# Optimization experiments

Hardware: AMD Instinct MI355X
Metric: run time of the kernel (lower is better)

The kernel has to match this reference:

```python
import jax, jax.numpy as jnp
import numpy as np

D_MODEL = 1024
N_HEADS = 16
D_FF = 4096
EPS = 1e-5


def layer_norm(x, gamma, beta):
    mu = jnp.mean(x, axis=-1, keepdims=True)
    var = jnp.mean(jnp.square(x - mu), axis=-1, keepdims=True)
    return (x - mu) * jax.lax.rsqrt(var + EPS) * gamma + beta


def setup_inputs() -> dict:
    key = jax.random.key(0)
    ks = jax.random.split(key, 12)
    C, F = D_MODEL, D_FF
    s = 1.0 / np.sqrt(C)
    sf = 1.0 / np.sqrt(F)
    return {
        "src": jax.random.normal(ks[0], (2, 2048, C), dtype=jnp.float32),
        "w_qkv": jax.random.uniform(ks[1], (3 * C, C), jnp.float32, -s, s),  # qkv_bias=False
        "w_proj": jax.random.uniform(ks[2], (C, C), jnp.float32, -s, s),
        "b_proj": jax.random.uniform(ks[3], (C,), jnp.float32, -s, s),
        "w1": jax.random.uniform(ks[4], (F, C), jnp.float32, -s, s),
        "b1": jax.random.uniform(ks[5], (F,), jnp.float32, -s, s),
        "w2": jax.random.uniform(ks[6], (C, F), jnp.float32, -sf, sf),
        "b2": jax.random.uniform(ks[7], (C,), jnp.float32, -sf, sf),
        "g1": jnp.ones((C,), jnp.float32),
        "be1": jnp.zeros((C,), jnp.float32),
        "g2": jnp.ones((C,), jnp.float32),
        "be2": jnp.zeros((C,), jnp.float32),
    }


def reference(src, w_qkv, w_proj, b_proj, w1, b1, w2, b2, g1, be1, g2, be2):
    B, N, C = src.shape
    H = N_HEADS
    D = C // H
    scale = D ** -0.5
    # --- self-attention (manual QK^T softmax) ---
    qkv = (src @ w_qkv.T).reshape(B, N, 3, H, D).transpose(2, 0, 3, 1, 4)  # [3,B,H,N,D]
    q, k, v = qkv[0], qkv[1], qkv[2]
    attn = jax.nn.softmax(jnp.einsum('bhnd,bhmd->bhnm', q, k) * scale, axis=-1)
    out = jnp.einsum('bhnm,bhmd->bhnd', attn, v).transpose(0, 2, 1, 3).reshape(B, N, C)
    out = out @ w_proj.T + b_proj
    # post-norm residual
    x = layer_norm(src + out, g1, be1)
    # --- FFN ---
    ff = jax.nn.relu(x @ w1.T + b1) @ w2.T + b2
    return layer_norm(x + ff, g2, be2)
```

## Files before the change

kernel.cpp:

```cpp
#include <hip/hip_runtime.h>
#include <hip/hip_bf16.h>
#include <stdint.h>

#define TOKENS 4096
#define SEQ    2048
#define CMODEL 1024
#define HEADS  16
#define HDIM   64
#define DFF    4096
#define NT     (SEQ / 64)

typedef __attribute__((ext_vector_type(8))) short     short8;
typedef __attribute__((ext_vector_type(8))) unsigned short ushort8;
typedef __attribute__((ext_vector_type(4))) unsigned short ushort4v;
typedef __attribute__((ext_vector_type(4))) float     f32x4;

typedef const __attribute__((address_space(1))) void gbl_cvoid;
typedef __attribute__((address_space(3))) void lds_void;

__device__ inline unsigned short f2bf(float f) {
  unsigned int u = __builtin_bit_cast(unsigned int, f);
  u += 0x7fffu + ((u >> 16) & 1u);
  return (unsigned short)(u >> 16);
}
__device__ inline float bf2f(unsigned short h) {
  unsigned int u = ((unsigned int)h) << 16;
  return __builtin_bit_cast(float, u);
}

__device__ inline void gload_lds16(const unsigned short* g, unsigned short* lds) {
  __builtin_amdgcn_global_load_lds((gbl_cvoid*)g, (lds_void*)lds, 16, 0, 0);
}

#define CVT_B0 524288
#define CVT_B1 917504
#define CVT_B2 1048576
#define CVT_B3 1572864
#define CVT_B4 2097152
__global__ __launch_bounds__(256) void k_cvt_all(
    const float* __restrict__ src, const float* __restrict__ wqkv,
    const float* __restrict__ wproj, const float* __restrict__ w1,
    const float* __restrict__ w2,
    unsigned short* __restrict__ o_src, unsigned short* __restrict__ o_wqkv,
    unsigned short* __restrict__ o_wproj, unsigned short* __restrict__ o_w1,
    unsigned short* __restrict__ o_w2)
{
  const int i = blockIdx.x * 256 + threadIdx.x;
  const float* in;
  unsigned short* out;
  int off;
  if (i < CVT_B0)      { in = src;   out = o_src;   off = i; }
  else if (i < CVT_B1) { in = wqkv;  out = o_wqkv;  off = i - CVT_B0; }
  else if (i < CVT_B2) { in = wproj; out = o_wproj; off = i - CVT_B1; }
  else if (i < CVT_B3) { in = w1;    out = o_w1;    off = i - CVT_B2; }
  else                 { in = w2;    out = o_w2;    off = i - CVT_B3; }
  const float4* p = (const float4*)in + 2 * (size_t)off;
  float4 a = p[0], b = p[1];
  ushort8 o;
  o[0] = f2bf(a.x); o[1] = f2bf(a.y); o[2] = f2bf(a.z); o[3] = f2bf(a.w);
  o[4] = f2bf(b.x); o[5] = f2bf(b.y); o[6] = f2bf(b.z); o[7] = f2bf(b.w);
  ((ushort8*)out)[off] = o;
}

template<int EPI>
__global__ __launch_bounds__(256) void k_gemm_bt(
    const unsigned short* __restrict__ A,
    const unsigned short* __restrict__ B,
    unsigned short* __restrict__ Cb,
    float* __restrict__ Cf,
    const float* __restrict__ bias,
    int M, int N, int K, int kspan)
{
  __shared__ unsigned short As[3][128 * 32];
  __shared__ unsigned short Bs[3][128 * 32];
  const int t = threadIdx.x;
  const int lane = t & 63;
  const int w = t >> 6;
  const int wr = w >> 1, wc = w & 1;
  const int nwg = gridDim.x * gridDim.y;
  const int bid = blockIdx.y * gridDim.x + blockIdx.x;
  const int swz = (bid & 7) * (nwg >> 3) + (bid >> 3);
  const int n0 = (swz % gridDim.x) * 128;
  const int m0 = (swz / gridDim.x) * 128;
  const int kbase = blockIdx.z * kspan;

  const int e0 = w * 1024 + lane * 8;
  const int e1 = e0 + 512;
  const int r0 = e0 >> 5, c0 = e0 & 31;
  const int r1 = e1 >> 5, c1 = e1 & 31;

  f32x4 acc[4][4] = {};
  const int lr = lane & 15, lh = lane >> 4;
  const int nkt = kspan >> 5;

  auto stage = [&](int kt, int buf) {
    const int kb = kbase + (kt << 5);
    gload_lds16(A + (size_t)(m0 + r0) * K + kb + c0, &As[buf][w * 1024]);
    gload_lds16(A + (size_t)(m0 + r1) * K + kb + c1, &As[buf][w * 1024 + 512]);
    gload_lds16(B + (size_t)(n0 + r0) * K + kb + c0, &Bs[buf][w * 1024]);
    gload_lds16(B + (size_t)(n0 + r1) * K + kb + c1, &Bs[buf][w * 1024 + 512]);
  };
  stage(0, 0);
  if (nkt > 1) stage(1, 1);

  int buf = 0;
  for (int kt = 0; kt < nkt; ++kt) {
    if (kt + 2 < nkt) {
      const int nb = buf + 2 >= 3 ? buf - 1 : buf + 2;
      stage(kt + 2, nb);
      asm volatile("s_waitcnt vmcnt(8)" ::: "memory");
    } else if (kt + 1 < nkt) {
      asm volatile("s_waitcnt vmcnt(4)" ::: "memory");
    } else {
      asm volatile("s_waitcnt vmcnt(0)" ::: "memory");
    }
    __builtin_amdgcn_s_barrier();
    __builtin_amdgcn_sched_barrier(0);
    short8 af[4], bg[4];
#pragma unroll
    for (int m = 0; m < 4; ++m)
      af[m] = *(const short8*)&As[buf][(wr * 64 + m * 16 + lr) * 32 + lh * 8];
#pragma unroll
    for (int n = 0; n < 4; ++n)
      bg[n] = *(const short8*)&Bs[buf][(wc * 64 + n * 16 + lr) * 32 + lh * 8];
#pragma unroll
    for (int m = 0; m < 4; ++m)
#pragma unroll
      for (int n = 0; n < 4; ++n)
        acc[m][n] = __builtin_amdgcn_mfma_f32_16x16x32_bf16(af[m], bg[n], acc[m][n], 0, 0, 0);
    __builtin_amdgcn_s_barrier();
    __builtin_amdgcn_sched_barrier(0);
    buf = buf + 1 >= 3 ? 0 : buf + 1;
  }

  float* Cfp = (EPI == 4) ? Cf + (size_t)blockIdx.z * ((size_t)M * N) : Cf;
  for (int m = 0; m < 4; ++m) {
    for (int n = 0; n < 4; ++n) {
      const int col = n0 + wc * 64 + n * 16 + lr;
      for (int r = 0; r < 4; ++r) {
        const int row = m0 + wr * 64 + m * 16 + lh * 4 + r;
        const size_t idx = (size_t)row * N + col;
        float v = acc[m][n][r];
        if (EPI == 0) {
          Cb[idx] = f2bf(v);
        } else if (EPI == 2) {
          v += bias[col];
          Cb[idx] = f2bf(v > 0.f ? v : 0.f);
        } else {
          Cfp[idx] = v;
        }
      }
    }
  }
}

__global__ __launch_bounds__(256) void k_attn(
    const unsigned short* __restrict__ qk,
    const unsigned short* __restrict__ vT,
    unsigned short* __restrict__ outb)
{
  __shared__ unsigned short Qs[64 * 64];
  __shared__ unsigned short Ks[2][64 * 64];
  __shared__ unsigned short Vt[2][64 * 64];
  __shared__ unsigned short Ps[4][16 * 72];

  const int t = threadIdx.x, lane = t & 63, w = t >> 6;
  const int bid0 = blockIdx.y * 32 + blockIdx.x;
  const int swz = (bid0 & 7) * 128 + (bid0 >> 3);
  const int bh = swz >> 5;
  const int b = bh >> 4, h = bh & 15;
  const int q0 = (swz & 31) * 64;
  const size_t tokbase = (size_t)b * SEQ;
  const int qoff = h * 64, koff = 1024 + h * 64;
  const size_t vbase = (size_t)(h * 64) * TOKENS + tokbase;
  const int lr = lane & 15, lh = lane >> 4, lh4 = lh * 4;

  const int srow = lane >> 3;
  const int scol = (((lane & 7) ^ srow) & 7) << 3;

  gload_lds16(qk + (tokbase + q0 + w * 16 + srow) * 2048 + qoff + scol, &Qs[w * 1024]);
  gload_lds16(qk + (tokbase + q0 + w * 16 + 8 + srow) * 2048 + qoff + scol, &Qs[w * 1024 + 512]);
  gload_lds16(qk + (tokbase + w * 16 + srow) * 2048 + koff + scol, &Ks[0][w * 1024]);
  gload_lds16(qk + (tokbase + w * 16 + 8 + srow) * 2048 + koff + scol, &Ks[0][w * 1024 + 512]);
  gload_lds16(vT + vbase + (size_t)(w * 16 + srow) * TOKENS + scol, &Vt[0][w * 1024]);
  gload_lds16(vT + vbase + (size_t)(w * 16 + 8 + srow) * TOKENS + scol, &Vt[0][w * 1024 + 512]);
  asm volatile("s_waitcnt vmcnt(0)" ::: "memory");
  __builtin_amdgcn_s_barrier();
  __builtin_amdgcn_sched_barrier(0);

  const int qrow = w * 16 + lr;
  const short8 aq0 = *(const short8*)&Qs[qrow * 64 + (((lh ^ (lr & 7)) & 7) << 3)];
  const short8 aq1 = *(const short8*)&Qs[qrow * 64 + ((((lh + 4) ^ (lr & 7)) & 7) << 3)];

  int koffs0[4], koffs1[4], voffs0[4], voffs1[4];
  for (int nf = 0; nf < 4; ++nf) {
    const int krow = nf * 16 + lr;
    koffs0[nf] = krow * 64 + (((lh ^ (lr & 7)) & 7) << 3);
    koffs1[nf] = krow * 64 + ((((lh + 4) ^ (lr & 7)) & 7) << 3);
    voffs0[nf] = koffs0[nf];
    voffs1[nf] = koffs1[nf];
  }
  const unsigned short* pa0p = &Ps[w][lr * 72 + lh * 8];
  const unsigned short* pa1p = &Ps[w][lr * 72 + 32 + lh * 8];

  float m_run = -1e30f, l_run = 0.f;
  f32x4 oacc[4] = {};
  const float SCL = 0.125f * 1.44269504089f;

#define ATTN_STEP(CUR, KT)                                                        \
  {                                                                               \
    const int ktn = (KT) + 1;                                                     \
    if (ktn < NT) {                                                               \
      gload_lds16(qk + (tokbase + ktn * 64 + w * 16 + srow) * 2048 + koff + scol, \
                  &Ks[1 - (CUR)][w * 1024]);                                      \
      gload_lds16(qk + (tokbase + ktn * 64 + w * 16 + 8 + srow) * 2048 + koff + scol,\
                  &Ks[1 - (CUR)][w * 1024 + 512]);                                \
      gload_lds16(vT + vbase + ktn * 64 + (size_t)(w * 16 + srow) * TOKENS + scol,\
                  &Vt[1 - (CUR)][w * 1024]);                                      \
      gload_lds16(vT + vbase + ktn * 64 + (size_t)(w * 16 + 8 + srow) * TOKENS + scol,\
                  &Vt[1 - (CUR)][w * 1024 + 512]);                                \
      asm volatile("s_waitcnt vmcnt(4)" ::: "memory");                            \
    } else {                                                                      \
      asm volatile("s_waitcnt vmcnt(0)" ::: "memory");                            \
    }                                                                             \
    __builtin_amdgcn_s_barrier();                                                 \
    __builtin_amdgcn_sched_barrier(0);                                            \
    f32x4 sacc[4] = {};                                                           \
    __builtin_amdgcn_s_setprio(1);                                                \
    for (int nf = 0; nf < 4; ++nf) {                                              \
      short8 bk0 = *(const short8*)&Ks[CUR][koffs0[nf]];                          \
      short8 bk1 = *(const short8*)&Ks[CUR][koffs1[nf]];                          \
      sacc[nf] = __builtin_amdgcn_mfma_f32_16x16x32_bf16(bk0, aq0, sacc[nf], 0, 0, 0);\
      sacc[nf] = __builtin_amdgcn_mfma_f32_16x16x32_bf16(bk1, aq1, sacc[nf], 0, 0, 0);\
    }                                                                             \
    __builtin_amdgcn_s_setprio(0);                                                \
    float a0 = fmaxf(fmaxf(sacc[0][0], sacc[0][1]), sacc[0][2]);                  \
    float a1 = fmaxf(fmaxf(sacc[0][3], sacc[1][0]), sacc[1][1]);                  \
    float a2 = fmaxf(fmaxf(sacc[1][2], sacc[1][3]), sacc[2][0]);                  \
    float a3 = fmaxf(fmaxf(sacc[2][1], sacc[2][2]), sacc[2][3]);                  \
    float a4 = fmaxf(fmaxf(sacc[3][0], sacc[3][1]), sacc[3][2]);                  \
    float tm = fmaxf(fmaxf(fmaxf(a0, a1), fmaxf(a2, a3)), fmaxf(a4, sacc[3][3])); \
    tm *= SCL;                                                                    \
    tm = fmaxf(tm, __shfl_xor(tm, 16));                                           \
    tm = fmaxf(tm, __shfl_xor(tm, 32));                                           \
    if (__any(tm > m_run + 5.f)) {               \
      const float mnew = fmaxf(m_run, tm);                                        \
      const float alpha = exp2f(m_run - mnew);                                    \
      m_run = mnew; l_run *= alpha;                                               \
      const float ar0 = __shfl(alpha, lh4 + 0), ar1 = __shfl(alpha, lh4 + 1);     \
      const float ar2 = __shfl(alpha, lh4 + 2), ar3 = __shfl(alpha, lh4 + 3);     \
      for (int nf = 0; nf < 4; ++nf) {                                            \
        oacc[nf][0] *= ar0; oacc[nf][1] *= ar1;                                   \
        oacc[nf][2] *= ar2; oacc[nf][3] *= ar3;                                   \
      }                                                                           \
    }                                                                             \
    float rs = 0.f;                                                               \
    for (int nf = 0; nf < 4; ++nf) {                                              \
      float p0 = exp2f(__builtin_fmaf(sacc[nf][0], SCL, -m_run));                 \
      float p1 = exp2f(__builtin_fmaf(sacc[nf][1], SCL, -m_run));                 \
      float p2 = exp2f(__builtin_fmaf(sacc[nf][2], SCL, -m_run));                 \
      float p3 = exp2f(__builtin_fmaf(sacc[nf][3], SCL, -m_run));                 \
      rs += (p0 + p1) + (p2 + p3);                                                \
      unsigned pk0, pk1;                                                          \
      asm("v_cvt_pk_bf16_f32 %0, %1, %2" : "=v"(pk0) : "v"(p0), "v"(p1));         \
      asm("v_cvt_pk_bf16_f32 %0, %1, %2" : "=v"(pk1) : "v"(p2), "v"(p3));         \
      uint2 pw; pw.x = pk0; pw.y = pk1;                                           \
      *(uint2*)&Ps[w][lr * 72 + nf * 16 + lh4] = pw;                              \
    }                                                                             \
    rs += __shfl_xor(rs, 16);                                                     \
    rs += __shfl_xor(rs, 32);                                                     \
    l_run += rs;                                                                  \
    short8 pa0 = *(const short8*)pa0p;                                            \
    short8 pa1 = *(const short8*)pa1p;                                            \
    __builtin_amdgcn_s_setprio(1);                                                \
    for (int nf = 0; nf < 4; ++nf) {                                              \
      short8 vb0 = *(const short8*)&Vt[CUR][voffs0[nf]];                          \
      short8 vb1 = *(const short8*)&Vt[CUR][voffs1[nf]];                          \
      oacc[nf] = __builtin_amdgcn_mfma_f32_16x16x32_bf16(pa0, vb0, oacc[nf], 0, 0, 0);\
      oacc[nf] = __builtin_amdgcn_mfma_f32_16x16x32_bf16(pa1, vb1, oacc[nf], 0, 0, 0);\
    }                                                                             \
    __builtin_amdgcn_s_setprio(0);                                                \
    __builtin_amdgcn_s_barrier();            \
    __builtin_amdgcn_sched_barrier(0);                                            \
  }

  for (int kt2 = 0; kt2 < NT; kt2 += 2) {
    ATTN_STEP(0, kt2)
    ATTN_STEP(1, kt2 + 1)
  }
#undef ATTN_STEP

  const float lf0 = __shfl(l_run, lh4 + 0);
  const float lf1 = __shfl(l_run, lh4 + 1);
  const float lf2 = __shfl(l_run, lh4 + 2);
  const float lf3 = __shfl(l_run, lh4 + 3);
  const float ri0 = 1.f / lf0, ri1 = 1.f / lf1, ri2 = 1.f / lf2, ri3 = 1.f / lf3;
  for (int nf = 0; nf < 4; ++nf) {
    const int col = h * 64 + nf * 16 + lr;
    const size_t rowb = (tokbase + q0 + w * 16 + lh4) * (size_t)CMODEL + col;
    outb[rowb]               = f2bf(oacc[nf][0] * ri0);
    outb[rowb + CMODEL]      = f2bf(oacc[nf][1] * ri1);
    outb[rowb + 2 * CMODEL]  = f2bf(oacc[nf][2] * ri2);
    outb[rowb + 3 * CMODEL]  = f2bf(oacc[nf][3] * ri3);
  }
}

__global__ __launch_bounds__(256) void k_ln1(
    const float* __restrict__ p,
    const float* __restrict__ src, const float* __restrict__ bias,
    const float* __restrict__ g, const float* __restrict__ b,
    unsigned short* __restrict__ xout)
{
  const int row = blockIdx.x;
  const int t = threadIdx.x;
  const size_t rb = (size_t)row * CMODEL;
  const float4 a0 = ((const float4*)(p + rb))[t];
  const float4 a1 = ((const float4*)(p + (size_t)TOKENS * CMODEL + rb))[t];
  const float4 sv = ((const float4*)(src + rb))[t];
  const float4 bb = ((const float4*)bias)[t];
  float4 v;
  v.x = a0.x + a1.x + sv.x + bb.x;
  v.y = a0.y + a1.y + sv.y + bb.y;
  v.z = a0.z + a1.z + sv.z + bb.z;
  v.w = a0.w + a1.w + sv.w + bb.w;
  float s  = v.x + v.y + v.z + v.w;
  float s2 = v.x * v.x + v.y * v.y + v.z * v.z + v.w * v.w;
  for (int off = 32; off; off >>= 1) { s += __shfl_down(s, off); s2 += __shfl_down(s2, off); }
  __shared__ float red[8];
  __shared__ float stats[2];
  const int wv = t >> 6;
  if ((t & 63) == 0) { red[wv] = s; red[4 + wv] = s2; }
  __syncthreads();
  if (t == 0) {
    float ts  = red[0] + red[1] + red[2] + red[3];
    float ts2 = red[4] + red[5] + red[6] + red[7];
    float mu  = ts * (1.f / CMODEL);
    float var = ts2 * (1.f / CMODEL) - mu * mu;
    stats[0] = mu; stats[1] = rsqrtf(var + 1e-5f);
  }
  __syncthreads();
  const float mu = stats[0], rstd = stats[1];
  float4 gv = ((const float4*)g)[t];
  float4 bv = ((const float4*)b)[t];
  ushort4v o;
  o[0] = f2bf((v.x - mu) * rstd * gv.x + bv.x);
  o[1] = f2bf((v.y - mu) * rstd * gv.y + bv.y);
  o[2] = f2bf((v.z - mu) * rstd * gv.z + bv.z);
  o[3] = f2bf((v.w - mu) * rstd * gv.w + bv.w);
  ((ushort4v*)(xout + rb))[t] = o;
}

__global__ __launch_bounds__(256) void k_ln2(
    const float* __restrict__ q,
    const unsigned short* __restrict__ xres, const float* __restrict__ bias,
    const float* __restrict__ g, const float* __restrict__ b,
    float* __restrict__ out)
{
  const int row = blockIdx.x;
  const int t = threadIdx.x;
  const size_t rb = (size_t)row * CMODEL;
  const float4 a0 = ((const float4*)(q + rb))[t];
  const float4 a1 = ((const float4*)(q + (size_t)TOKENS * CMODEL + rb))[t];
  const ushort4v xv = ((const ushort4v*)(xres + rb))[t];
  const float4 bb = ((const float4*)bias)[t];
  float4 v;
  v.x = a0.x + a1.x + bf2f(xv[0]) + bb.x;
  v.y = a0.y + a1.y + bf2f(xv[1]) + bb.y;
  v.z = a0.z + a1.z + bf2f(xv[2]) + bb.z;
  v.w = a0.w + a1.w + bf2f(xv[3]) + bb.w;
  float s  = v.x + v.y + v.z + v.w;
  float s2 = v.x * v.x + v.y * v.y + v.z * v.z + v.w * v.w;
  for (int off = 32; off; off >>= 1) { s += __shfl_down(s, off); s2 += __shfl_down(s2, off); }
  __shared__ float red[8];
  __shared__ float stats[2];
  const int wv = t >> 6;
  if ((t & 63) == 0) { red[wv] = s; red[4 + wv] = s2; }
  __syncthreads();
  if (t == 0) {
    float ts  = red[0] + red[1] + red[2] + red[3];
    float ts2 = red[4] + red[5] + red[6] + red[7];
    float mu  = ts * (1.f / CMODEL);
    float var = ts2 * (1.f / CMODEL) - mu * mu;
    stats[0] = mu; stats[1] = rsqrtf(var + 1e-5f);
  }
  __syncthreads();
  const float mu = stats[0], rstd = stats[1];
  float4 gv = ((const float4*)g)[t];
  float4 bv = ((const float4*)b)[t];
  float4 o;
  o.x = (v.x - mu) * rstd * gv.x + bv.x;
  o.y = (v.y - mu) * rstd * gv.y + bv.y;
  o.z = (v.z - mu) * rstd * gv.z + bv.z;
  o.w = (v.w - mu) * rstd * gv.w + bv.w;
  ((float4*)(out + rb))[t] = o;
}

extern "C" void kernel_launch(void* const* d_in, const int* in_sizes, int n_in,
                              void* d_out, int out_size, void* d_ws, size_t ws_size,
                              hipStream_t stream) {
  const float* src    = (const float*)d_in[0];
  const float* w_qkv  = (const float*)d_in[1];
  const float* w_proj = (const float*)d_in[2];
  const float* b_proj = (const float*)d_in[3];
  const float* w1     = (const float*)d_in[4];
  const float* b1     = (const float*)d_in[5];
  const float* w2     = (const float*)d_in[6];
  const float* b2     = (const float*)d_in[7];
  const float* g1     = (const float*)d_in[8];
  const float* be1    = (const float*)d_in[9];
  const float* g2     = (const float*)d_in[10];
  const float* be2    = (const float*)d_in[11];
  float* out = (float*)d_out;

  char* ws = (char*)d_ws;
  size_t off = 0;
  auto alloc = [&](size_t bytes) -> void* {
    void* p = ws + off;
    off += (bytes + 255) & ~(size_t)255;
    return p;
  };
  unsigned short* src_bf   = (unsigned short*)alloc((size_t)TOKENS * CMODEL * 2);
  unsigned short* wqkv_bf  = (unsigned short*)alloc((size_t)3 * CMODEL * CMODEL * 2);
  unsigned short* wproj_bf = (unsigned short*)alloc((size_t)CMODEL * CMODEL * 2);
  unsigned short* w1_bf    = (unsigned short*)alloc((size_t)DFF * CMODEL * 2);
  unsigned short* w2_bf    = (unsigned short*)alloc((size_t)CMODEL * DFF * 2);
  unsigned short* x_bf     = (unsigned short*)alloc((size_t)TOKENS * CMODEL * 2);
  unsigned short* h_bf     = (unsigned short*)alloc((size_t)TOKENS * DFF * 2);
  char* regionR = (char*)alloc((size_t)64 * 1024 * 1024);
  unsigned short* qk_bf    = (unsigned short*)regionR;
  unsigned short* vT_bf    = (unsigned short*)(regionR + (size_t)TOKENS * 2048 * 2);
  unsigned short* attno_bf = (unsigned short*)(regionR + (size_t)TOKENS * 2048 * 2
                                                       + (size_t)CMODEL * TOKENS * 2);
  float*          p_proj   = (float*)(regionR + (size_t)TOKENS * 2048 * 2
                                              + (size_t)CMODEL * TOKENS * 2
                                              + (size_t)TOKENS * CMODEL * 2);
  float*          p_ffn2   = (float*)regionR;

  k_cvt_all<<<CVT_B4 / 256, 256, 0, stream>>>(src, w_qkv, w_proj, w1, w2,
      src_bf, wqkv_bf, wproj_bf, w1_bf, w2_bf);
  k_gemm_bt<0><<<dim3(2048 / 128, TOKENS / 128), 256, 0, stream>>>(
      src_bf, wqkv_bf, qk_bf, nullptr, nullptr, TOKENS, 2048, CMODEL, CMODEL);
  k_gemm_bt<0><<<dim3(TOKENS / 128, CMODEL / 128), 256, 0, stream>>>(
      wqkv_bf + (size_t)2048 * CMODEL, src_bf, vT_bf, nullptr, nullptr,
      CMODEL, TOKENS, CMODEL, CMODEL);
  k_attn<<<dim3(SEQ / 64, 2 * HEADS), 256, 0, stream>>>(qk_bf, vT_bf, attno_bf);
  k_gemm_bt<4><<<dim3(CMODEL / 128, TOKENS / 128, 2), 256, 0, stream>>>(
      attno_bf, wproj_bf, nullptr, p_proj, nullptr, TOKENS, CMODEL, CMODEL, CMODEL / 2);
  k_ln1<<<TOKENS, 256, 0, stream>>>(p_proj, src, b_proj, g1, be1, x_bf);
  k_gemm_bt<2><<<dim3(DFF / 128, TOKENS / 128), 256, 0, stream>>>(
      x_bf, w1_bf, h_bf, nullptr, b1, TOKENS, DFF, CMODEL, CMODEL);
  k_gemm_bt<4><<<dim3(CMODEL / 128, TOKENS / 128, 2), 256, 0, stream>>>(
      h_bf, w2_bf, nullptr, p_ffn2, nullptr, TOKENS, CMODEL, DFF, DFF / 2);
  k_ln2<<<TOKENS, 256, 0, stream>>>(p_ffn2, x_bf, b2, g2, be2, out);
}
```

Before: 400.7 us.

## Replace split-K GEMMs with BN=64 tiles and fuse bias+residual into epilogue

The N=1024 GEMMs (attention projection and FFN down) drop split-K over z=2 and use 128x64 tiles instead, which keeps the grid at 512 blocks. Bias and residual addition move into the GEMM epilogue so the layernorm kernels only read one fp32 buffer, and ln1 and ln2 become a single templated kernel. In attention the Q staging buffer is reused for the P tile to reduce LDS use. This removes the second partial-sum write and read, at the cost of narrower tiles with lower reuse and a full-K loop per block.

```diff
diff --git a/kernel.cpp b/kernel.cpp
--- a/kernel.cpp
+++ b/kernel.cpp
@@ -62,17 +62,20 @@
   ((ushort8*)out)[off] = o;
 }
 
-template<int EPI>
+template<int EPI, int BN>
 __global__ __launch_bounds__(256) void k_gemm_bt(
     const unsigned short* __restrict__ A,
     const unsigned short* __restrict__ B,
     unsigned short* __restrict__ Cb,
     float* __restrict__ Cf,
     const float* __restrict__ bias,
-    int M, int N, int K, int kspan)
+    const float* __restrict__ resf,
+    const unsigned short* __restrict__ resb,
+    int M, int N, int K)
 {
+  constexpr int NF = BN >> 5;
   __shared__ unsigned short As[3][128 * 32];
-  __shared__ unsigned short Bs[3][128 * 32];
+  __shared__ unsigned short Bs[3][BN * 32];
   const int t = threadIdx.x;
   const int lane = t & 63;
   const int w = t >> 6;
@@ -80,25 +83,30 @@
   const int nwg = gridDim.x * gridDim.y;
   const int bid = blockIdx.y * gridDim.x + blockIdx.x;
   const int swz = (bid & 7) * (nwg >> 3) + (bid >> 3);
-  const int n0 = (swz % gridDim.x) * 128;
+  const int n0 = (swz % gridDim.x) * BN;
   const int m0 = (swz / gridDim.x) * 128;
-  const int kbase = blockIdx.z * kspan;
 
   const int e0 = w * 1024 + lane * 8;
   const int e1 = e0 + 512;
   const int r0 = e0 >> 5, c0 = e0 & 31;
   const int r1 = e1 >> 5, c1 = e1 & 31;
-
-  f32x4 acc[4][4] = {};
+  const int eB = w * 512 + lane * 8;
+  const int rB = eB >> 5, cB = eB & 31;
+
+  f32x4 acc[4][NF] = {};
   const int lr = lane & 15, lh = lane >> 4;
-  const int nkt = kspan >> 5;
+  const int nkt = K >> 5;
 
   auto stage = [&](int kt, int buf) {
-    const int kb = kbase + (kt << 5);
+    const int kb = kt << 5;
     gload_lds16(A + (size_t)(m0 + r0) * K + kb + c0, &As[buf][w * 1024]);
     gload_lds16(A + (size_t)(m0 + r1) * K + kb + c1, &As[buf][w * 1024 + 512]);
-    gload_lds16(B + (size_t)(n0 + r0) * K + kb + c0, &Bs[buf][w * 1024]);
-    gload_lds16(B + (size_t)(n0 + r1) * K + kb + c1, &Bs[buf][w * 1024 + 512]);
+    if constexpr (BN == 128) {
+      gload_lds16(B + (size_t)(n0 + r0) * K + kb + c0, &Bs[buf][w * 1024]);
+      gload_lds16(B + (size_t)(n0 + r1) * K + kb + c1, &Bs[buf][w * 1024 + 512]);
+    } else {
+      gload_lds16(B + (size_t)(n0 + rB) * K + kb + cB, &Bs[buf][w * 512]);
+    }
   };
   stage(0, 0);
   if (nkt > 1) stage(1, 1);
@@ -108,46 +116,49 @@
     if (kt + 2 < nkt) {
       const int nb = buf + 2 >= 3 ? buf - 1 : buf + 2;
       stage(kt + 2, nb);
-      asm volatile("s_waitcnt vmcnt(8)" ::: "memory");
+      if constexpr (BN == 128) asm volatile("s_waitcnt vmcnt(8)" ::: "memory");
+      else                     asm volatile("s_waitcnt vmcnt(6)" ::: "memory");
     } else if (kt + 1 < nkt) {
-      asm volatile("s_waitcnt vmcnt(4)" ::: "memory");
+      if constexpr (BN == 128) asm volatile("s_waitcnt vmcnt(4)" ::: "memory");
+      else                     asm volatile("s_waitcnt vmcnt(3)" ::: "memory");
     } else {
       asm volatile("s_waitcnt vmcnt(0)" ::: "memory");
     }
     __builtin_amdgcn_s_barrier();
     __builtin_amdgcn_sched_barrier(0);
-    short8 af[4], bg[4];
+    short8 af[4], bg[NF];
 #pragma unroll
     for (int m = 0; m < 4; ++m)
       af[m] = *(const short8*)&As[buf][(wr * 64 + m * 16 + lr) * 32 + lh * 8];
 #pragma unroll
-    for (int n = 0; n < 4; ++n)
-      bg[n] = *(const short8*)&Bs[buf][(wc * 64 + n * 16 + lr) * 32 + lh * 8];
+    for (int n = 0; n < NF; ++n)
+      bg[n] = *(const short8*)&Bs[buf][(wc * (BN / 2) + n * 16 + lr) * 32 + lh * 8];
 #pragma unroll
     for (int m = 0; m < 4; ++m)
 #pragma unroll
-      for (int n = 0; n < 4; ++n)
+      for (int n = 0; n < NF; ++n)
         acc[m][n] = __builtin_amdgcn_mfma_f32_16x16x32_bf16(af[m], bg[n], acc[m][n], 0, 0, 0);
     __builtin_amdgcn_s_barrier();
     __builtin_amdgcn_sched_barrier(0);
     buf = buf + 1 >= 3 ? 0 : buf + 1;
   }
 
-  float* Cfp = (EPI == 4) ? Cf + (size_t)blockIdx.z * ((size_t)M * N) : Cf;
   for (int m = 0; m < 4; ++m) {
-    for (int n = 0; n < 4; ++n) {
-      const int col = n0 + wc * 64 + n * 16 + lr;
+    for (int n = 0; n < NF; ++n) {
+      const int col = n0 + wc * (BN / 2) + n * 16 + lr;
       for (int r = 0; r < 4; ++r) {
         const int row = m0 + wr * 64 + m * 16 + lh * 4 + r;
         const size_t idx = (size_t)row * N + col;
         float v = acc[m][n][r];
         if (EPI == 0) {
           Cb[idx] = f2bf(v);
+        } else if (EPI == 1) {
+          Cf[idx] = v + bias[col] + resf[idx];
         } else if (EPI == 2) {
           v += bias[col];
           Cb[idx] = f2bf(v > 0.f ? v : 0.f);
         } else {
-          Cfp[idx] = v;
+          Cf[idx] = v + bias[col] + bf2f(resb[idx]);
         }
       }
     }
@@ -159,10 +170,9 @@
     const unsigned short* __restrict__ vT,
     unsigned short* __restrict__ outb)
 {
-  __shared__ unsigned short Qs[64 * 64];
   __shared__ unsigned short Ks[2][64 * 64];
   __shared__ unsigned short Vt[2][64 * 64];
-  __shared__ unsigned short Ps[4][16 * 72];
+  __shared__ unsigned short QPs[4 * 1024];
 
   const int t = threadIdx.x, lane = t & 63, w = t >> 6;
   const int bid0 = blockIdx.y * 32 + blockIdx.x;
@@ -178,8 +188,8 @@
   const int srow = lane >> 3;
   const int scol = (((lane & 7) ^ srow) & 7) << 3;
 
-  gload_lds16(qk + (tokbase + q0 + w * 16 + srow) * 2048 + qoff + scol, &Qs[w * 1024]);
-  gload_lds16(qk + (tokbase + q0 + w * 16 + 8 + srow) * 2048 + qoff + scol, &Qs[w * 1024 + 512]);
+  gload_lds16(qk + (tokbase + q0 + w * 16 + srow) * 2048 + qoff + scol, &QPs[w * 1024]);
+  gload_lds16(qk + (tokbase + q0 + w * 16 + 8 + srow) * 2048 + qoff + scol, &QPs[w * 1024 + 512]);
   gload_lds16(qk + (tokbase + w * 16 + srow) * 2048 + koff + scol, &Ks[0][w * 1024]);
   gload_lds16(qk + (tokbase + w * 16 + 8 + srow) * 2048 + koff + scol, &Ks[0][w * 1024 + 512]);
   gload_lds16(vT + vbase + (size_t)(w * 16 + srow) * TOKENS + scol, &Vt[0][w * 1024]);
@@ -188,20 +198,20 @@
   __builtin_amdgcn_s_barrier();
   __builtin_amdgcn_sched_barrier(0);
 
-  const int qrow = w * 16 + lr;
-  const short8 aq0 = *(const short8*)&Qs[qrow * 64 + (((lh ^ (lr & 7)) & 7) << 3)];
-  const short8 aq1 = *(const short8*)&Qs[qrow * 64 + ((((lh + 4) ^ (lr & 7)) & 7) << 3)];
-
-  int koffs0[4], koffs1[4], voffs0[4], voffs1[4];
+  const short8 aq0 = *(const short8*)&QPs[w * 1024 + lr * 64 + (((lh ^ (lr & 7)) & 7) << 3)];
+  const short8 aq1 = *(const short8*)&QPs[w * 1024 + lr * 64 + ((((lh + 4) ^ (lr & 7)) & 7) << 3)];
+
+  int koffs0[4], koffs1[4];
   for (int nf = 0; nf < 4; ++nf) {
     const int krow = nf * 16 + lr;
     koffs0[nf] = krow * 64 + (((lh ^ (lr & 7)) & 7) << 3);
     koffs1[nf] = krow * 64 + ((((lh + 4) ^ (lr & 7)) & 7) << 3);
-    voffs0[nf] = koffs0[nf];
-    voffs1[nf] = koffs1[nf];
-  }
-  const unsigned short* pa0p = &Ps[w][lr * 72 + lh * 8];
-  const unsigned short* pa1p = &Ps[w][lr * 72 + 32 + lh * 8];
+  }
+  const unsigned short* pa0p = &QPs[w * 1024 + lr * 64 + (((lh ^ (lr & 7)) & 7) << 3)];
+  const unsigned short* pa1p = &QPs[w * 1024 + lr * 64 + ((((4 + lh) ^ (lr & 7)) & 7) << 3)];
+  int pwr[4];
+  for (int nf = 0; nf < 4; ++nf)
+    pwr[nf] = w * 1024 + lr * 64 + ((((nf * 2 + (lh4 >> 3)) ^ (lr & 7)) & 7) << 3) + (lh4 & 7);
 
   float m_run = -1e30f, l_run = 0.f;
   f32x4 oacc[4] = {};
@@ -265,7 +275,7 @@
       asm("v_cvt_pk_bf16_f32 %0, %1, %2" : "=v"(pk0) : "v"(p0), "v"(p1));         \
       asm("v_cvt_pk_bf16_f32 %0, %1, %2" : "=v"(pk1) : "v"(p2), "v"(p3));         \
       uint2 pw; pw.x = pk0; pw.y = pk1;                                           \
-      *(uint2*)&Ps[w][lr * 72 + nf * 16 + lh4] = pw;                              \
+      *(uint2*)&QPs[pwr[nf]] = pw;                                                \
     }                                                                             \
     rs += __shfl_xor(rs, 16);                                                     \
     rs += __shfl_xor(rs, 32);                                                     \
@@ -274,8 +284,8 @@
     short8 pa1 = *(const short8*)pa1p;                                            \
     __builtin_amdgcn_s_setprio(1);                                                \
     for (int nf = 0; nf < 4; ++nf) {                                              \
-      short8 vb0 = *(const short8*)&Vt[CUR][voffs0[nf]];                          \
-      short8 vb1 = *(const short8*)&Vt[CUR][voffs1[nf]];                          \
+      short8 vb0 = *(const short8*)&Vt[CUR][koffs0[nf]];                          \
+      short8 vb1 = *(const short8*)&Vt[CUR][koffs1[nf]];                          \
       oacc[nf] = __builtin_amdgcn_mfma_f32_16x16x32_bf16(pa0, vb0, oacc[nf], 0, 0, 0);\
       oacc[nf] = __builtin_amdgcn_mfma_f32_16x16x32_bf16(pa1, vb1, oacc[nf], 0, 0, 0);\
     }                                                                             \
@@ -305,24 +315,15 @@
   }
 }
 
-__global__ __launch_bounds__(256) void k_ln1(
-    const float* __restrict__ p,
-    const float* __restrict__ src, const float* __restrict__ bias,
+template<int OUT_BF>
+__global__ __launch_bounds__(256) void k_ln(const float* __restrict__ in,
     const float* __restrict__ g, const float* __restrict__ b,
-    unsigned short* __restrict__ xout)
+    float* __restrict__ outf, unsigned short* __restrict__ outb)
 {
   const int row = blockIdx.x;
   const int t = threadIdx.x;
-  const size_t rb = (size_t)row * CMODEL;
-  const float4 a0 = ((const float4*)(p + rb))[t];
-  const float4 a1 = ((const float4*)(p + (size_t)TOKENS * CMODEL + rb))[t];
-  const float4 sv = ((const float4*)(src + rb))[t];
-  const float4 bb = ((const float4*)bias)[t];
-  float4 v;
-  v.x = a0.x + a1.x + sv.x + bb.x;
-  v.y = a0.y + a1.y + sv.y + bb.y;
-  v.z = a0.z + a1.z + sv.z + bb.z;
-  v.w = a0.w + a1.w + sv.w + bb.w;
+  const float4* x4 = (const float4*)(in + (size_t)row * CMODEL);
+  float4 v = x4[t];
   float s  = v.x + v.y + v.z + v.w;
   float s2 = v.x * v.x + v.y * v.y + v.z * v.z + v.w * v.w;
   for (int off = 32; off; off >>= 1) { s += __shfl_down(s, off); s2 += __shfl_down(s2, off); }
@@ -342,57 +343,17 @@
   const float mu = stats[0], rstd = stats[1];
   float4 gv = ((const float4*)g)[t];
   float4 bv = ((const float4*)b)[t];
-  ushort4v o;
-  o[0] = f2bf((v.x - mu) * rstd * gv.x + bv.x);
-  o[1] = f2bf((v.y - mu) * rstd * gv.y + bv.y);
-  o[2] = f2bf((v.z - mu) * rstd * gv.z + bv.z);
-  o[3] = f2bf((v.w - mu) * rstd * gv.w + bv.w);
-  ((ushort4v*)(xout + rb))[t] = o;
-}
-
-__global__ __launch_bounds__(256) void k_ln2(
-    const float* __restrict__ q,
-    const unsigned short* __restrict__ xres, const float* __restrict__ bias,
-    const float* __restrict__ g, const float* __restrict__ b,
-    float* __restrict__ out)
-{
-  const int row = blockIdx.x;
-  const int t = threadIdx.x;
-  const size_t rb = (size_t)row * CMODEL;
-  const float4 a0 = ((const float4*)(q + rb))[t];
-  const float4 a1 = ((const float4*)(q + (size_t)TOKENS * CMODEL + rb))[t];
-  const ushort4v xv = ((const ushort4v*)(xres + rb))[t];
-  const float4 bb = ((const float4*)bias)[t];
-  float4 v;
-  v.x = a0.x + a1.x + bf2f(xv[0]) + bb.x;
-  v.y = a0.y + a1.y + bf2f(xv[1]) + bb.y;
-  v.z = a0.z + a1.z + bf2f(xv[2]) + bb.z;
-  v.w = a0.w + a1.w + bf2f(xv[3]) + bb.w;
-  float s  = v.x + v.y + v.z + v.w;
-  float s2 = v.x * v.x + v.y * v.y + v.z * v.z + v.w * v.w;
-  for (int off = 32; off; off >>= 1) { s += __shfl_down(s, off); s2 += __shfl_down(s2, off); }
-  __shared__ float red[8];
-  __shared__ float stats[2];
-  const int wv = t >> 6;
-  if ((t & 63) == 0) { red[wv] = s; red[4 + wv] = s2; }
-  __syncthreads();
-  if (t == 0) {
-    float ts  = red[0] + red[1] + red[2] + red[3];
-    float ts2 = red[4] + red[5] + red[6] + red[7];
-    float mu  = ts * (1.f / CMODEL);
-    float var = ts2 * (1.f / CMODEL) - mu * mu;
-    stats[0] = mu; stats[1] = rsqrtf(var + 1e-5f);
-  }
-  __syncthreads();
-  const float mu = stats[0], rstd = stats[1];
-  float4 gv = ((const float4*)g)[t];
-  float4 bv = ((const float4*)b)[t];
-  float4 o;
-  o.x = (v.x - mu) * rstd * gv.x + bv.x;
-  o.y = (v.y - mu) * rstd * gv.y + bv.y;
-  o.z = (v.z - mu) * rstd * gv.z + bv.z;
-  o.w = (v.w - mu) * rstd * gv.w + bv.w;
-  ((float4*)(out + rb))[t] = o;
+  float o0 = (v.x - mu) * rstd * gv.x + bv.x;
+  float o1 = (v.y - mu) * rstd * gv.y + bv.y;
+  float o2 = (v.z - mu) * rstd * gv.z + bv.z;
+  float o3 = (v.w - mu) * rstd * gv.w + bv.w;
+  if (OUT_BF) {
+    ushort4v o; o[0] = f2bf(o0); o[1] = f2bf(o1); o[2] = f2bf(o2); o[3] = f2bf(o3);
+    ((ushort4v*)(outb + (size_t)row * CMODEL))[t] = o;
+  } else {
+    float4 o; o.x = o0; o.y = o1; o.z = o2; o.w = o3;
+    ((float4*)(outf + (size_t)row * CMODEL))[t] = o;
+  }
 }
 
 extern "C" void kernel_launch(void* const* d_in, const int* in_sizes, int n_in,
@@ -426,30 +387,25 @@
   unsigned short* w2_bf    = (unsigned short*)alloc((size_t)CMODEL * DFF * 2);
   unsigned short* x_bf     = (unsigned short*)alloc((size_t)TOKENS * CMODEL * 2);
   unsigned short* h_bf     = (unsigned short*)alloc((size_t)TOKENS * DFF * 2);
-  char* regionR = (char*)alloc((size_t)64 * 1024 * 1024);
-  unsigned short* qk_bf    = (unsigned short*)regionR;
-  unsigned short* vT_bf    = (unsigned short*)(regionR + (size_t)TOKENS * 2048 * 2);
-  unsigned short* attno_bf = (unsigned short*)(regionR + (size_t)TOKENS * 2048 * 2
-                                                       + (size_t)CMODEL * TOKENS * 2);
-  float*          p_proj   = (float*)(regionR + (size_t)TOKENS * 2048 * 2
-                                              + (size_t)CMODEL * TOKENS * 2
-                                              + (size_t)TOKENS * CMODEL * 2);
-  float*          p_ffn2   = (float*)regionR;
+  unsigned short* qk_bf    = (unsigned short*)alloc((size_t)TOKENS * 2048 * 2);
+  unsigned short* vT_bf    = (unsigned short*)alloc((size_t)CMODEL * TOKENS * 2);
+  unsigned short* attno_bf = (unsigned short*)alloc((size_t)TOKENS * CMODEL * 2);
+  float*          z_f32    = (float*)alloc((size_t)TOKENS * CMODEL * 4);
 
   k_cvt_all<<<CVT_B4 / 256, 256, 0, stream>>>(src, w_qkv, w_proj, w1, w2,
       src_bf, wqkv_bf, wproj_bf, w1_bf, w2_bf);
-  k_gemm_bt<0><<<dim3(2048 / 128, TOKENS / 128), 256, 0, stream>>>(
-      src_bf, wqkv_bf, qk_bf, nullptr, nullptr, TOKENS, 2048, CMODEL, CMODEL);
-  k_gemm_bt<0><<<dim3(TOKENS / 128, CMODEL / 128), 256, 0, stream>>>(
-      wqkv_bf + (size_t)2048 * CMODEL, src_bf, vT_bf, nullptr, nullptr,
-      CMODEL, TOKENS, CMODEL, CMODEL);
+  k_gemm_bt<0, 128><<<dim3(2048 / 128, TOKENS / 128), 256, 0, stream>>>(
+      src_bf, wqkv_bf, qk_bf, nullptr, nullptr, nullptr, nullptr, TOKENS, 2048, CMODEL);
+  k_gemm_bt<0, 128><<<dim3(TOKENS / 128, CMODEL / 128), 256, 0, stream>>>(
+      wqkv_bf + (size_t)2048 * CMODEL, src_bf, vT_bf, nullptr, nullptr, nullptr, nullptr,
+      CMODEL, TOKENS, CMODEL);
   k_attn<<<dim3(SEQ / 64, 2 * HEADS), 256, 0, stream>>>(qk_bf, vT_bf, attno_bf);
-  k_gemm_bt<4><<<dim3(CMODEL / 128, TOKENS / 128, 2), 256, 0, stream>>>(
-      attno_bf, wproj_bf, nullptr, p_proj, nullptr, TOKENS, CMODEL, CMODEL, CMODEL / 2);
-  k_ln1<<<TOKENS, 256, 0, stream>>>(p_proj, src, b_proj, g1, be1, x_bf);
-  k_gemm_bt<2><<<dim3(DFF / 128, TOKENS / 128), 256, 0, stream>>>(
-      x_bf, w1_bf, h_bf, nullptr, b1, TOKENS, DFF, CMODEL, CMODEL);
-  k_gemm_bt<4><<<dim3(CMODEL / 128, TOKENS / 128, 2), 256, 0, stream>>>(
-      h_bf, w2_bf, nullptr, p_ffn2, nullptr, TOKENS, CMODEL, DFF, DFF / 2);
-  k_ln2<<<TOKENS, 256, 0, stream>>>(p_ffn2, x_bf, b2, g2, be2, out);
-}
+  k_gemm_bt<1, 64><<<dim3(CMODEL / 64, TOKENS / 128), 256, 0, stream>>>(
+      attno_bf, wproj_bf, nullptr, z_f32, b_proj, src, nullptr, TOKENS, CMODEL, CMODEL);
+  k_ln<1><<<TOKENS, 256, 0, stream>>>(z_f32, g1, be1, nullptr, x_bf);
+  k_gemm_bt<2, 128><<<dim3(DFF / 128, TOKENS / 128), 256, 0, stream>>>(
+      x_bf, w1_bf, h_bf, nullptr, b1, nullptr, nullptr, TOKENS, DFF, CMODEL);
+  k_gemm_bt<3, 64><<<dim3(CMODEL / 64, TOKENS / 128), 256, 0, stream>>>(
+      h_bf, w2_bf, nullptr, z_f32, b2, nullptr, x_bf, TOKENS, CMODEL, DFF);
+  k_ln<0><<<TOKENS, 256, 0, stream>>>(z_f32, g2, be2, out, nullptr);
+}
```

New measurement: 396.1 us. Within noise of the previous version (-1.2%).
